# Kernel optimization log

Measured on AMD Instinct MI355X. Metric: run time of the kernel, lower is better.

The kernel has to match this reference:

```python
import jax, jax.numpy as jnp
import numpy as np

B = 32768
K = 8           # moe_num_experts
LATENT = 256    # latent_dim
COND = 1024     # fusion_hidden_dim
HID = 128       # moe_expert_hidden_dim
EIN = LATENT + COND + 1  # expert input dim = 1281


def setup_inputs() -> dict:
    key = jax.random.key(0)
    ks = jax.random.split(key, 12)
    cond = jax.random.normal(ks[0], (B, COND), dtype=jnp.float32)
    u = jax.random.normal(ks[1], (B, LATENT), dtype=jnp.float32)
    tau = jax.random.uniform(ks[2], (B, 1), dtype=jnp.float32)
    # posterior gate: positive, sums to 1 over K (realistic p_hat)
    p_raw = jax.random.uniform(ks[3], (B, K), dtype=jnp.float32)
    p_hat = p_raw / jnp.sum(p_raw, axis=-1, keepdims=True)
    s = 0.02
    W1 = jax.random.normal(ks[4], (K, EIN, HID), dtype=jnp.float32) * s
    b1 = jnp.zeros((K, HID), dtype=jnp.float32)
    W2 = jax.random.normal(ks[5], (K, HID, HID), dtype=jnp.float32) * s
    b2 = jnp.zeros((K, HID), dtype=jnp.float32)
    W3 = jax.random.normal(ks[6], (K, HID, LATENT), dtype=jnp.float32) * s
    b3 = jnp.zeros((K, LATENT), dtype=jnp.float32)
    return {"cond": cond, "u": u, "tau": tau, "p_hat": p_hat,
            "W1": W1, "b1": b1, "W2": W2, "b2": b2, "W3": W3, "b3": b3}


def reference(cond, u, tau, p_hat, W1, b1, W2, b2, W3, b3):
    # Training path: gate = p_hat (no smooth switching, no running gate).
    x = jnp.concatenate([u, cond, tau], axis=-1)           # (B, EIN)
    h = jax.nn.silu(jnp.einsum('bd,kdh->bkh', x, W1) + b1) # (B, K, HID)
    h = jax.nn.silu(jnp.einsum('bkh,khg->bkg', h, W2) + b2)
    v_experts = jnp.einsum('bkg,kgl->bkl', h, W3) + b3     # (B, K, LATENT)
    v = jnp.einsum('bk,bkl->bl', p_hat, v_experts)         # (B, LATENT)
    return v
```

## Files before the change

kernel.cpp:

```cpp
#include <hip/hip_runtime.h>
#include <stdint.h>

typedef unsigned short u16;
typedef __attribute__((ext_vector_type(8))) short short8;
typedef __attribute__((ext_vector_type(4))) float f32x4;
typedef __attribute__((ext_vector_type(4))) uint32_t u32x4;

#define KEXP   8
#define LATENT 256
#define CONDD  1024
#define HID    128
#define EIN    1281
#define EINP   1344
#define NCH    21
#define NTOT   1024
#define BROWS  32768

__device__ __forceinline__ u16 f2bf(float x) {
  uint32_t v = __float_as_uint(x);
  v += 0x7fffu + ((v >> 16) & 1u);
  return (u16)(v >> 16);
}

__device__ __forceinline__ void async16(const void* g, void* l) {
  __builtin_amdgcn_global_load_lds(
      (const __attribute__((address_space(1))) void*)g,
      (__attribute__((address_space(3))) void*)l, 16, 0, 0);
}

__device__ __forceinline__ float silu(float x) { return x / (1.f + __expf(-x)); }

#define W1_TILES (KEXP * 42 * 4)
#define W2_TILES (KEXP * 4 * 4)
#define W3_TILES (KEXP * 4 * 8)
#define WCONV_TILES (W1_TILES + W2_TILES + W3_TILES)
#define XGRP (BROWS * 168)
#define XBLK (XGRP / 256)

__global__ __launch_bounds__(256)
void prep(const float* __restrict__ W1, const float* __restrict__ W2,
          const float* __restrict__ W3, const float* __restrict__ cond,
          const float* __restrict__ uu, const float* __restrict__ tau,
          u16* __restrict__ W1t, u16* __restrict__ W2t, u16* __restrict__ W3t2,
          u16* __restrict__ Xbf) {
  __shared__ float t[32][33];
  const int bid = blockIdx.x;
  if (bid >= WCONV_TILES) {
    int g = (bid - WCONV_TILES) * 256 + threadIdx.x;
    int row = g / 168;
    int c8  = g - row * 168;
    float f0 = 0.f, f1 = 0.f, f2 = 0.f, f3 = 0.f, f4 = 0.f, f5 = 0.f, f6 = 0.f, f7 = 0.f;
    if (c8 < 32) {
      const float4* p = (const float4*)(uu + (size_t)row * LATENT + c8 * 8);
      float4 a = p[0], b = p[1];
      f0 = a.x; f1 = a.y; f2 = a.z; f3 = a.w; f4 = b.x; f5 = b.y; f6 = b.z; f7 = b.w;
    } else if (c8 < 160) {
      const float4* p = (const float4*)(cond + (size_t)row * CONDD + (c8 - 32) * 8);
      float4 a = p[0], b = p[1];
      f0 = a.x; f1 = a.y; f2 = a.z; f3 = a.w; f4 = b.x; f5 = b.y; f6 = b.z; f7 = b.w;
    } else if (c8 == 160) {
      f0 = tau[row];
    }
    u32x4 pk;
    pk[0] = (uint32_t)f2bf(f0) | ((uint32_t)f2bf(f1) << 16);
    pk[1] = (uint32_t)f2bf(f2) | ((uint32_t)f2bf(f3) << 16);
    pk[2] = (uint32_t)f2bf(f4) | ((uint32_t)f2bf(f5) << 16);
    pk[3] = (uint32_t)f2bf(f6) | ((uint32_t)f2bf(f7) << 16);
    *(u32x4*)(Xbf + (size_t)row * EINP + c8 * 8) = pk;
    return;
  }
  const int tx = threadIdx.x & 31, ty = threadIdx.x >> 5;
  if (bid < W1_TILES) {
    int k = bid / 168, r = bid % 168;
    int d0 = (r / 4) * 32, h0 = (r % 4) * 32;
    const float* src = W1 + (size_t)k * EIN * HID;
    #pragma unroll
    for (int s = 0; s < 4; ++s) {
      int d = d0 + ty + s * 8;
      t[ty + s * 8][tx] = (d < EIN) ? src[(size_t)d * HID + h0 + tx] : 0.f;
    }
    __syncthreads();
    u16* dst = W1t + (size_t)k * HID * EINP;
    #pragma unroll
    for (int s = 0; s < 4; ++s)
      dst[(size_t)(h0 + ty + s * 8) * EINP + d0 + tx] = f2bf(t[tx][ty + s * 8]);
  } else if (bid < W1_TILES + W2_TILES) {
    int j = bid - W1_TILES;
    int k = j / 16, r = j % 16;
    int d0 = (r / 4) * 32, h0 = (r % 4) * 32;
    const float* src = W2 + (size_t)k * HID * HID;
    #pragma unroll
    for (int s = 0; s < 4; ++s)
      t[ty + s * 8][tx] = src[(size_t)(d0 + ty + s * 8) * HID + h0 + tx];
    __syncthreads();
    u16* dst = W2t + (size_t)k * HID * HID;
    #pragma unroll
    for (int s = 0; s < 4; ++s)
      dst[(size_t)(h0 + ty + s * 8) * HID + d0 + tx] = f2bf(t[tx][ty + s * 8]);
  } else {
    int j = bid - W1_TILES - W2_TILES;
    int k = j / 32, r = j % 32;
    int d0 = (r / 8) * 32, h0 = (r % 8) * 32;
    const float* src = W3 + (size_t)k * HID * LATENT;
    #pragma unroll
    for (int s = 0; s < 4; ++s)
      t[ty + s * 8][tx] = src[(size_t)(d0 + ty + s * 8) * LATENT + h0 + tx];
    __syncthreads();
    #pragma unroll
    for (int s = 0; s < 4; ++s)
      W3t2[(size_t)(h0 + ty + s * 8) * NTOT + k * HID + d0 + tx] = f2bf(t[tx][ty + s * 8]);
  }
}

__global__ __launch_bounds__(256, 2)
void h1_fused(const u16* __restrict__ Xbf, const u16* __restrict__ W1t,
              const float* __restrict__ b1, const u16* __restrict__ W2t,
              const float* __restrict__ b2, const float* __restrict__ p_hat,
              u16* __restrict__ H) {
  __shared__ struct {
    union {
      struct { u16 As[2][128 * 64]; u16 Bs[2][128 * 64]; } s;
      struct { u16 As2[128 * 128]; u16 Bs2[2][128 * 64]; } g;
      u16 Cs[128 * 72];
    } u;
    float Ps[128];
  } sm;

  const int tid  = threadIdx.x;
  const int wave = tid >> 6;
  const int lane = tid & 63;
  const int q    = lane >> 4;
  const int ln   = lane & 15;
  const int wm   = wave >> 1, wn = wave & 1;
  const int bid  = blockIdx.x;
  const int mt   = ((bid >> 6) << 3) | (bid & 7);
  const int e    = (bid >> 3) & 7;
  const int m0   = mt * 128;
  const u16* w1k = W1t + (size_t)e * HID * EINP;
  const u16* xtb = Xbf + (size_t)m0 * EINP;

  if (tid < 128) sm.Ps[tid] = p_hat[(size_t)(m0 + tid) * KEXP + e];

  const f32x4 fz = {0.f, 0.f, 0.f, 0.f};
  f32x4 acc[4][4];
  #pragma unroll
  for (int m = 0; m < 4; ++m)
    #pragma unroll
    for (int n = 0; n < 4; ++n) acc[m][n] = fz;

  const int rloc = lane >> 3;
  const int gsw  = lane & 7;
  const int gsrc = gsw ^ rloc;

  auto stage = [&](int d0, int bf) {
    #pragma unroll
    for (int i = 0; i < 4; ++i) {
      int rbase = (wave * 4 + i) * 8;
      async16(xtb + (size_t)(rbase + rloc) * EINP + d0 + gsrc * 8,
              &sm.u.s.As[bf][rbase * 64]);
      async16(w1k + (size_t)(rbase + rloc) * EINP + d0 + gsrc * 8,
              &sm.u.s.Bs[bf][rbase * 64]);
    }
  };
  auto mfma_chunk = [&](int bf) {
    const u16* Ab = sm.u.s.As[bf];
    const u16* Bb = sm.u.s.Bs[bf];
    __builtin_amdgcn_s_setprio(1);
    #pragma unroll
    for (int ks = 0; ks < 2; ++ks) {
      short8 a[4], b[4];
      #pragma unroll
      for (int m = 0; m < 4; ++m) {
        int r = wm * 64 + m * 16 + ln;
        int g = (ks * 4 + q) ^ (r & 7);
        a[m] = *(const short8*)(&Ab[r * 64 + g * 8]);
      }
      #pragma unroll
      for (int n = 0; n < 4; ++n) {
        int c = wn * 64 + n * 16 + ln;
        int g = (ks * 4 + q) ^ (c & 7);
        b[n] = *(const short8*)(&Bb[c * 64 + g * 8]);
      }
      #pragma unroll
      for (int m = 0; m < 4; ++m)
        #pragma unroll
        for (int n = 0; n < 4; ++n)
          acc[m][n] = __builtin_amdgcn_mfma_f32_16x16x32_bf16(a[m], b[n], acc[m][n], 0, 0, 0);
    }
    __builtin_amdgcn_s_setprio(0);
  };

  stage(0, 0);
  asm volatile("s_waitcnt vmcnt(0)" ::: "memory");
  __builtin_amdgcn_s_barrier();
  __builtin_amdgcn_sched_barrier(0);

  #pragma unroll 1
  for (int ic2 = 0; ic2 < 10; ++ic2) {
    const int d = ic2 * 128;
    stage(d + 64, 1);
    mfma_chunk(0);
    asm volatile("s_waitcnt vmcnt(0)" ::: "memory");
    __builtin_amdgcn_s_barrier();
    __builtin_amdgcn_sched_barrier(0);
    stage(d + 128, 0);
    mfma_chunk(1);
    asm volatile("s_waitcnt vmcnt(0)" ::: "memory");
    __builtin_amdgcn_s_barrier();
    __builtin_amdgcn_sched_barrier(0);
  }
  mfma_chunk(0);
  __syncthreads();

  const u16* w2k = W2t + (size_t)e * HID * HID;
  #pragma unroll
  for (int kc = 0; kc < 2; ++kc)
    #pragma unroll
    for (int i = 0; i < 4; ++i) {
      int rbase = (wave * 4 + i) * 8;
      async16(w2k + (size_t)(rbase + rloc) * HID + kc * 64 + gsrc * 8,
              &sm.u.g.Bs2[kc][rbase * 64]);
    }

  #pragma unroll
  for (int n = 0; n < 4; ++n) {
    int cl = wn * 64 + n * 16 + ln;
    float bv = b1[e * HID + cl];
    #pragma unroll
    for (int m = 0; m < 4; ++m)
      #pragma unroll
      for (int r = 0; r < 4; ++r) {
        int row = wm * 64 + m * 16 + q * 4 + r;
        sm.u.g.As2[row * 128 + (((cl >> 3) ^ (row & 7)) << 3) + (cl & 7)] =
            f2bf(silu(acc[m][n][r] + bv));
      }
  }

  f32x4 acc2[4][4];
  #pragma unroll
  for (int m = 0; m < 4; ++m)
    #pragma unroll
    for (int n = 0; n < 4; ++n) acc2[m][n] = fz;

  __syncthreads();

  #pragma unroll
  for (int kc = 0; kc < 2; ++kc) {
    #pragma unroll
    for (int ks = 0; ks < 2; ++ks) {
      short8 a[4], b[4];
      #pragma unroll
      for (int m = 0; m < 4; ++m) {
        int r = wm * 64 + m * 16 + ln;
        int G = kc * 8 + ks * 4 + q;
        int g = (G & 8) | ((G ^ (r & 7)) & 7);
        a[m] = *(const short8*)(&sm.u.g.As2[r * 128 + g * 8]);
      }
      #pragma unroll
      for (int n = 0; n < 4; ++n) {
        int c = wn * 64 + n * 16 + ln;
        int g = (ks * 4 + q) ^ (c & 7);
        b[n] = *(const short8*)(&sm.u.g.Bs2[kc][c * 64 + g * 8]);
      }
      #pragma unroll
      for (int m = 0; m < 4; ++m)
        #pragma unroll
        for (int n = 0; n < 4; ++n)
          acc2[m][n] = __builtin_amdgcn_mfma_f32_16x16x32_bf16(a[m], b[n], acc2[m][n], 0, 0, 0);
    }
  }
  __syncthreads();

  u16* hb = H + (size_t)m0 * NTOT + e * HID;
  #pragma unroll 1
  for (int hf = 0; hf < 2; ++hf) {
    if (wn == hf) {
      #pragma unroll
      for (int n = 0; n < 4; ++n) {
        int cl = n * 16 + ln;
        float bv = b2[e * HID + hf * 64 + cl];
        #pragma unroll
        for (int m = 0; m < 4; ++m)
          #pragma unroll
          for (int r = 0; r < 4; ++r) {
            int row = wm * 64 + m * 16 + q * 4 + r;
            sm.u.Cs[row * 72 + cl] = f2bf(sm.Ps[row] * silu(acc2[m][n][r] + bv));
          }
      }
    }
    __syncthreads();
    #pragma unroll
    for (int i = 0; i < 4; ++i) {
      int lin = tid + i * 256;
      int row = lin >> 3;
      int grp = lin & 7;
      *(u32x4*)(hb + (size_t)row * NTOT + hf * 64 + grp * 8) =
          *(const u32x4*)(&sm.u.Cs[row * 72 + grp * 8]);
    }
    __syncthreads();
  }
}

__global__ __launch_bounds__(256, 2)
void out_gemm(const u16* __restrict__ H, const float* __restrict__ p_hat,
              const u16* __restrict__ W3t2, const float* __restrict__ b3,
              float* __restrict__ out) {
  __shared__ struct {
    u16 As[2][64 * 64];
    u16 Bs[2][128 * 64];
    float Ps[64 * 8];
    float B3s[128 * 8];
  } sm;

  const int tid  = threadIdx.x;
  const int wave = tid >> 6;
  const int lane = tid & 63;
  const int q    = lane >> 4;
  const int ln   = lane & 15;
  const int bid  = blockIdx.x;
  const int mt   = ((bid >> 4) << 3) | (bid & 7);
  const int bn   = (bid >> 3) & 1;
  const int m0   = mt * 64, n0 = bn * 128;

  if (tid < 128) {
    int row = tid >> 1, h = tid & 1;
    *(float4*)(&sm.Ps[row * 8 + h * 4]) = *(const float4*)(p_hat + (size_t)(m0 + row) * KEXP + h * 4);
  }
  #pragma unroll
  for (int i = 0; i < 4; ++i) {
    int k = i * 2 + (tid >> 7);
    int c = tid & 127;
    sm.B3s[c * 8 + k] = b3[k * LATENT + n0 + c];
  }

  const f32x4 fz = {0.f, 0.f, 0.f, 0.f};
  f32x4 acc[4][2];
  #pragma unroll
  for (int m = 0; m < 4; ++m) { acc[m][0] = fz; acc[m][1] = fz; }

  const int rloc = lane >> 3;
  const int gsw  = lane & 7;
  const int gsrc = gsw ^ rloc;

  auto stage = [&](int d0, int bf) {
    #pragma unroll
    for (int i = 0; i < 2; ++i) {
      int rbase = (wave * 2 + i) * 8;
      async16(H + (size_t)(m0 + rbase + rloc) * NTOT + d0 + gsrc * 8,
              &sm.As[bf][rbase * 64]);
    }
    #pragma unroll
    for (int i = 0; i < 4; ++i) {
      int rbase = (wave * 4 + i) * 8;
      async16(W3t2 + (size_t)(n0 + rbase + rloc) * NTOT + d0 + gsrc * 8,
              &sm.Bs[bf][rbase * 64]);
    }
  };
  auto mfma_chunk = [&](int bf) {
    const u16* Ab = sm.As[bf];
    const u16* Bb = sm.Bs[bf];
    __builtin_amdgcn_s_setprio(1);
    #pragma unroll
    for (int ks = 0; ks < 2; ++ks) {
      short8 a[4], b[2];
      #pragma unroll
      for (int m = 0; m < 4; ++m) {
        int r = m * 16 + ln;
        int g = (ks * 4 + q) ^ (r & 7);
        a[m] = *(const short8*)(&Ab[r * 64 + g * 8]);
      }
      #pragma unroll
      for (int n = 0; n < 2; ++n) {
        int c = wave * 32 + n * 16 + ln;
        int g = (ks * 4 + q) ^ (c & 7);
        b[n] = *(const short8*)(&Bb[c * 64 + g * 8]);
      }
      #pragma unroll
      for (int m = 0; m < 4; ++m)
        #pragma unroll
        for (int n = 0; n < 2; ++n)
          acc[m][n] = __builtin_amdgcn_mfma_f32_16x16x32_bf16(a[m], b[n], acc[m][n], 0, 0, 0);
    }
    __builtin_amdgcn_s_setprio(0);
  };

  stage(0, 0);
  asm volatile("s_waitcnt vmcnt(0)" ::: "memory");
  __builtin_amdgcn_s_barrier();
  __builtin_amdgcn_sched_barrier(0);

  #pragma unroll 1
  for (int k2 = 0; k2 < 8; ++k2) {
    const int d = k2 * 128;
    stage(d + 64, 1);
    mfma_chunk(0);
    asm volatile("s_waitcnt vmcnt(0)" ::: "memory");
    __builtin_amdgcn_s_barrier();
    __builtin_amdgcn_sched_barrier(0);
    if (k2 < 7) {
      stage(d + 128, 0);
      mfma_chunk(1);
      asm volatile("s_waitcnt vmcnt(0)" ::: "memory");
      __builtin_amdgcn_s_barrier();
      __builtin_amdgcn_sched_barrier(0);
    }
  }
  mfma_chunk(1);

  #pragma unroll
  for (int n = 0; n < 2; ++n) {
    int col = wave * 32 + n * 16 + ln;
    float4 c0 = *(const float4*)(&sm.B3s[col * 8]);
    float4 c1 = *(const float4*)(&sm.B3s[col * 8 + 4]);
    #pragma unroll
    for (int m = 0; m < 4; ++m)
      #pragma unroll
      for (int r = 0; r < 4; ++r) {
        int row = m * 16 + q * 4 + r;
        float4 p0 = *(const float4*)(&sm.Ps[row * 8]);
        float4 p1 = *(const float4*)(&sm.Ps[row * 8 + 4]);
        float v = acc[m][n][r]
                + p0.x * c0.x + p0.y * c0.y + p0.z * c0.z + p0.w * c0.w
                + p1.x * c1.x + p1.y * c1.y + p1.z * c1.z + p1.w * c1.w;
        out[(size_t)(m0 + row) * LATENT + n0 + col] = v;
      }
  }
}

__global__ __launch_bounds__(256, 4)
void h1_gemm(const float* __restrict__ cond, const float* __restrict__ uu,
             const float* __restrict__ tau, const u16* __restrict__ W1t,
             const float* __restrict__ b1, u16* __restrict__ H1) {
  __shared__ union {
    struct { u16 As[128 * 64]; u16 Bs[128 * 64]; } s;
    u16 Cs[128 * 72];
  } sm;

  const int tid  = threadIdx.x;
  const int wave = tid >> 6;
  const int lane = tid & 63;
  const int q    = lane >> 4;
  const int ln   = lane & 15;
  const int wm   = wave >> 1, wn = wave & 1;
  const int bid  = blockIdx.x;
  const int mt   = ((bid >> 6) << 3) | (bid & 7);
  const int e    = (bid >> 3) & 7;
  const int m0   = mt * 128, n0 = e * 128;
  const u16* w1k = W1t + (size_t)e * HID * EINP;

  const f32x4 fz = {0.f, 0.f, 0.f, 0.f};
  f32x4 acc[4][4];
  #pragma unroll
  for (int m = 0; m < 4; ++m)
    #pragma unroll
    for (int n = 0; n < 4; ++n) acc[m][n] = fz;

  #pragma unroll 1
  for (int ic = 0; ic < NCH; ++ic) {
    const int d0 = ic * 64;
    #pragma unroll
    for (int i = 0; i < 4; ++i) {
      int lin  = tid + i * 256;
      int row  = lin >> 3;
      int gsw  = lin & 7;
      int gsrc = gsw ^ (row & 7);
      int gr   = m0 + row;
      float f0, f1, f2, f3, f4, f5, f6, f7;
      if (d0 < 256) {
        const float4* p = (const float4*)(uu + (size_t)gr * LATENT + d0 + gsrc * 8);
        float4 A = p[0], Bv = p[1];
        f0 = A.x; f1 = A.y; f2 = A.z; f3 = A.w; f4 = Bv.x; f5 = Bv.y; f6 = Bv.z; f7 = Bv.w;
      } else if (d0 < 1280) {
        const float4* p = (const float4*)(cond + (size_t)gr * CONDD + (d0 - 256) + gsrc * 8);
        float4 A = p[0], Bv = p[1];
        f0 = A.x; f1 = A.y; f2 = A.z; f3 = A.w; f4 = Bv.x; f5 = Bv.y; f6 = Bv.z; f7 = Bv.w;
      } else {
        float tv = tau[gr];
        f0 = (gsrc == 0) ? tv : 0.f;
        f1 = f2 = f3 = f4 = f5 = f6 = f7 = 0.f;
      }
      u32x4 pk;
      pk[0] = (uint32_t)f2bf(f0) | ((uint32_t)f2bf(f1) << 16);
      pk[1] = (uint32_t)f2bf(f2) | ((uint32_t)f2bf(f3) << 16);
      pk[2] = (uint32_t)f2bf(f4) | ((uint32_t)f2bf(f5) << 16);
      pk[3] = (uint32_t)f2bf(f6) | ((uint32_t)f2bf(f7) << 16);
      *(u32x4*)(&sm.s.As[row * 64 + gsw * 8]) = pk;
    }
    {
      int rloc = lane >> 3;
      int gsw  = lane & 7;
      int gsrc = gsw ^ rloc;
      #pragma unroll
      for (int i = 0; i < 4; ++i) {
        int rbase = (wave * 4 + i) * 8;
        async16(w1k + (size_t)(rbase + rloc) * EINP + d0 + gsrc * 8,
                &sm.s.Bs[rbase * 64]);
      }
    }
    __syncthreads();
    #pragma unroll
    for (int ks = 0; ks < 2; ++ks) {
      short8 a[4], b[4];
      #pragma unroll
      for (int m = 0; m < 4; ++m) {
        int r = wm * 64 + m * 16 + ln;
        int g = (ks * 4 + q) ^ (r & 7);
        a[m] = *(const short8*)(&sm.s.As[r * 64 + g * 8]);
      }
      #pragma unroll
      for (int n = 0; n < 4; ++n) {
        int c = wn * 64 + n * 16 + ln;
        int g = (ks * 4 + q) ^ (c & 7);
        b[n] = *(const short8*)(&sm.s.Bs[c * 64 + g * 8]);
      }
      #pragma unroll
      for (int m = 0; m < 4; ++m)
        #pragma unroll
        for (int n = 0; n < 4; ++n)
          acc[m][n] = __builtin_amdgcn_mfma_f32_16x16x32_bf16(a[m], b[n], acc[m][n], 0, 0, 0);
    }
    __syncthreads();
  }

  #pragma unroll 1
  for (int hf = 0; hf < 2; ++hf) {
    if (wn == hf) {
      #pragma unroll
      for (int n = 0; n < 4; ++n) {
        int cl = n * 16 + ln;
        float bv = b1[n0 + hf * 64 + cl];
        #pragma unroll
        for (int m = 0; m < 4; ++m)
          #pragma unroll
          for (int r = 0; r < 4; ++r)
            sm.Cs[(wm * 64 + m * 16 + q * 4 + r) * 72 + cl] = f2bf(silu(acc[m][n][r] + bv));
      }
    }
    __syncthreads();
    #pragma unroll
    for (int i = 0; i < 4; ++i) {
      int lin = tid + i * 256;
      int row = lin >> 3;
      int grp = lin & 7;
      *(u32x4*)(H1 + (size_t)(m0 + row) * NTOT + n0 + hf * 64 + grp * 8) =
          *(const u32x4*)(&sm.Cs[row * 72 + grp * 8]);
    }
    __syncthreads();
  }
}

__global__ __launch_bounds__(256, 4)
void h2_gemm(u16* __restrict__ H, const float* __restrict__ p_hat,
             const u16* __restrict__ W2t, const float* __restrict__ b2) {
  __shared__ struct {
    union { struct { u16 As[128 * 64]; u16 Bs[128 * 64]; } s; u16 Cs[128 * 72]; } u;
    float Ps[128];
  } sm;

  const int tid  = threadIdx.x;
  const int wave = tid >> 6;
  const int lane = tid & 63;
  const int q    = lane >> 4;
  const int ln   = lane & 15;
  const int wm   = wave >> 1, wn = wave & 1;
  const int mt   = blockIdx.x >> 3;
  const int e    = blockIdx.x & 7;
  const int row0 = mt * 128;

  if (tid < 128) sm.Ps[tid] = p_hat[(size_t)(row0 + tid) * KEXP + e];

  const u16* w2k = W2t + (size_t)e * HID * HID;
  u16* hb = H + (size_t)row0 * NTOT + e * HID;

  const f32x4 fz = {0.f, 0.f, 0.f, 0.f};
  f32x4 acc[4][4];
  #pragma unroll
  for (int m = 0; m < 4; ++m)
    #pragma unroll
    for (int n = 0; n < 4; ++n) acc[m][n] = fz;

  const int rloc = lane >> 3;
  const int gsw  = lane & 7;
  const int gsrc = gsw ^ rloc;

  #pragma unroll 1
  for (int kc = 0; kc < 2; ++kc) {
    #pragma unroll
    for (int i = 0; i < 4; ++i) {
      int rbase = (wave * 4 + i) * 8;
      async16(hb + (size_t)(rbase + rloc) * NTOT + kc * 64 + gsrc * 8,
              &sm.u.s.As[rbase * 64]);
      async16(w2k + (size_t)(rbase + rloc) * HID + kc * 64 + gsrc * 8,
              &sm.u.s.Bs[rbase * 64]);
    }
    __syncthreads();
    #pragma unroll
    for (int ks = 0; ks < 2; ++ks) {
      short8 a[4], b[4];
      #pragma unroll
      for (int m = 0; m < 4; ++m) {
        int r = wm * 64 + m * 16 + ln;
        int g = (ks * 4 + q) ^ (r & 7);
        a[m] = *(const short8*)(&sm.u.s.As[r * 64 + g * 8]);
      }
      #pragma unroll
      for (int n = 0; n < 4; ++n) {
        int c = wn * 64 + n * 16 + ln;
        int g = (ks * 4 + q) ^ (c & 7);
        b[n] = *(const short8*)(&sm.u.s.Bs[c * 64 + g * 8]);
      }
      #pragma unroll
      for (int m = 0; m < 4; ++m)
        #pragma unroll
        for (int n = 0; n < 4; ++n)
          acc[m][n] = __builtin_amdgcn_mfma_f32_16x16x32_bf16(a[m], b[n], acc[m][n], 0, 0, 0);
    }
    __syncthreads();
  }

  #pragma unroll 1
  for (int hf = 0; hf < 2; ++hf) {
    if (wn == hf) {
      #pragma unroll
      for (int n = 0; n < 4; ++n) {
        int cl = n * 16 + ln;
        float bv = b2[e * HID + hf * 64 + cl];
        #pragma unroll
        for (int m = 0; m < 4; ++m)
          #pragma unroll
          for (int r = 0; r < 4; ++r) {
            int row = wm * 64 + m * 16 + q * 4 + r;
            sm.u.Cs[row * 72 + cl] = f2bf(sm.Ps[row] * silu(acc[m][n][r] + bv));
          }
      }
    }
    __syncthreads();
    #pragma unroll
    for (int i = 0; i < 4; ++i) {
      int lin = tid + i * 256;
      int row = lin >> 3;
      int grp = lin & 7;
      *(u32x4*)(hb + (size_t)row * NTOT + hf * 64 + grp * 8) =
          *(const u32x4*)(&sm.u.Cs[row * 72 + grp * 8]);
    }
    __syncthreads();
  }
}

extern "C" void kernel_launch(void* const* d_in, const int* in_sizes, int n_in,
                              void* d_out, int out_size, void* d_ws, size_t ws_size,
                              hipStream_t stream) {
  const float* cond  = (const float*)d_in[0];
  const float* u     = (const float*)d_in[1];
  const float* tau   = (const float*)d_in[2];
  const float* p_hat = (const float*)d_in[3];
  const float* W1    = (const float*)d_in[4];
  const float* b1    = (const float*)d_in[5];
  const float* W2    = (const float*)d_in[6];
  const float* b2    = (const float*)d_in[7];
  const float* W3    = (const float*)d_in[8];
  const float* b3    = (const float*)d_in[9];
  float* out = (float*)d_out;

  const size_t N1 = (size_t)KEXP * HID * EINP;
  const size_t N2 = (size_t)KEXP * HID * HID;
  const size_t N3 = (size_t)LATENT * NTOT;
  const size_t NH = (size_t)BROWS * NTOT;
  const size_t NX = (size_t)BROWS * EINP;

  u16* W1t  = (u16*)d_ws;
  u16* W2t  = W1t + N1;
  u16* W3t2 = W2t + N2;
  u16* H    = W3t2 + N3;

  if (ws_size >= (N1 + N2 + N3 + NH + NX) * sizeof(u16)) {
    u16* Xbf = H + NH;
    prep<<<WCONV_TILES + XBLK, 256, 0, stream>>>(W1, W2, W3, cond, u, tau,
                                                 W1t, W2t, W3t2, Xbf);
    h1_fused<<<2048, 256, 0, stream>>>(Xbf, W1t, b1, W2t, b2, p_hat, H);
    out_gemm<<<1024, 256, 0, stream>>>(H, p_hat, W3t2, b3, out);
  } else if (ws_size >= (N1 + N2 + N3 + NH) * sizeof(u16)) {
    prep<<<WCONV_TILES, 256, 0, stream>>>(W1, W2, W3, cond, u, tau,
                                          W1t, W2t, W3t2, (u16*)nullptr);
    h1_gemm<<<2048, 256, 0, stream>>>(cond, u, tau, W1t, b1, H);
    h2_gemm<<<2048, 256, 0, stream>>>(H, p_hat, W2t, b2);
    out_gemm<<<1024, 256, 0, stream>>>(H, p_hat, W3t2, b3, out);
  }
}
```

Measured before the change: 431.7 us.

## Deepen async prefetch pipelines with triple buffering and partial vmcnt waits

```diff
diff --git a/kernel.cpp b/kernel.cpp
--- a/kernel.cpp
+++ b/kernel.cpp
@@ -117,13 +117,10 @@
               const float* __restrict__ b1, const u16* __restrict__ W2t,
               const float* __restrict__ b2, const float* __restrict__ p_hat,
               u16* __restrict__ H) {
-  __shared__ struct {
-    union {
-      struct { u16 As[2][128 * 64]; u16 Bs[2][128 * 64]; } s;
-      struct { u16 As2[128 * 128]; u16 Bs2[2][128 * 64]; } g;
-      u16 Cs[128 * 72];
-    } u;
-    float Ps[128];
+  __shared__ union {
+    struct { u16 As[3][8192]; u16 Bs[2][8192]; } s;
+    struct { u16 As2[16384]; u16 Bs2[2][8192]; } g;
+    u16 Cs[128 * 72];
   } sm;
 
   const int tid  = threadIdx.x;
@@ -139,8 +136,6 @@
   const u16* w1k = W1t + (size_t)e * HID * EINP;
   const u16* xtb = Xbf + (size_t)m0 * EINP;
 
-  if (tid < 128) sm.Ps[tid] = p_hat[(size_t)(m0 + tid) * KEXP + e];
-
   const f32x4 fz = {0.f, 0.f, 0.f, 0.f};
   f32x4 acc[4][4];
   #pragma unroll
@@ -152,19 +147,20 @@
   const int gsw  = lane & 7;
   const int gsrc = gsw ^ rloc;
 
-  auto stage = [&](int d0, int bf) {
-    #pragma unroll
-    for (int i = 0; i < 4; ++i) {
-      int rbase = (wave * 4 + i) * 8;
-      async16(xtb + (size_t)(rbase + rloc) * EINP + d0 + gsrc * 8,
-              &sm.u.s.As[bf][rbase * 64]);
-      async16(w1k + (size_t)(rbase + rloc) * EINP + d0 + gsrc * 8,
-              &sm.u.s.Bs[bf][rbase * 64]);
-    }
-  };
-  auto mfma_chunk = [&](int bf) {
-    const u16* Ab = sm.u.s.As[bf];
-    const u16* Bb = sm.u.s.Bs[bf];
+#define H1_SA(d0, buf) { \
+  _Pragma("unroll") \
+  for (int i_ = 0; i_ < 4; ++i_) { \
+    int rb_ = (wave * 4 + i_) * 8; \
+    async16(xtb + (size_t)(rb_ + rloc) * EINP + (d0) + gsrc * 8, &sm.s.As[buf][rb_ * 64]); \
+  } }
+#define H1_SB(d0, buf) { \
+  _Pragma("unroll") \
+  for (int i_ = 0; i_ < 4; ++i_) { \
+    int rb_ = (wave * 4 + i_) * 8; \
+    async16(w1k + (size_t)(rb_ + rloc) * EINP + (d0) + gsrc * 8, &sm.s.Bs[buf][rb_ * 64]); \
+  } }
+
+  auto mfma_chunk = [&](const u16* Ab, const u16* Bb) {
     __builtin_amdgcn_s_setprio(1);
     #pragma unroll
     for (int ks = 0; ks < 2; ++ks) {
@@ -190,26 +186,39 @@
     __builtin_amdgcn_s_setprio(0);
   };
 
-  stage(0, 0);
-  asm volatile("s_waitcnt vmcnt(0)" ::: "memory");
+#define H1_CH(trel, ac, bc, bp, ap, vm) \
+  H1_SB(db + ((trel) + 1) * 64, bp); \
+  H1_SA(db + ((trel) + 2) * 64, ap); \
+  mfma_chunk(sm.s.As[ac], sm.s.Bs[bc]); \
+  asm volatile("s_waitcnt vmcnt(" #vm ")" ::: "memory"); \
+  __builtin_amdgcn_s_barrier(); \
+  __builtin_amdgcn_sched_barrier(0);
+
+  H1_SA(0, 0); H1_SB(0, 0); H1_SA(64, 1);
+  asm volatile("s_waitcnt vmcnt(4)" ::: "memory");
   __builtin_amdgcn_s_barrier();
   __builtin_amdgcn_sched_barrier(0);
 
   #pragma unroll 1
-  for (int ic2 = 0; ic2 < 10; ++ic2) {
-    const int d = ic2 * 128;
-    stage(d + 64, 1);
-    mfma_chunk(0);
+  for (int j = 0; j < 3; ++j) {
+    const int db = j * 384;
+    H1_CH(0, 0, 0, 1, 2, 4)
+    H1_CH(1, 1, 1, 0, 0, 4)
+    H1_CH(2, 2, 0, 1, 1, 4)
+    H1_CH(3, 0, 1, 0, 2, 4)
+    H1_CH(4, 1, 0, 1, 0, 4)
+    H1_CH(5, 2, 1, 0, 1, 4)
+  }
+  {
+    const int db = 1152;
+    H1_CH(0, 0, 0, 1, 2, 4)
+    H1_SB(db + 128, 0);
+    mfma_chunk(sm.s.As[1], sm.s.Bs[1]);
     asm volatile("s_waitcnt vmcnt(0)" ::: "memory");
     __builtin_amdgcn_s_barrier();
     __builtin_amdgcn_sched_barrier(0);
-    stage(d + 128, 0);
-    mfma_chunk(1);
-    asm volatile("s_waitcnt vmcnt(0)" ::: "memory");
-    __builtin_amdgcn_s_barrier();
-    __builtin_amdgcn_sched_barrier(0);
-  }
-  mfma_chunk(0);
+    mfma_chunk(sm.s.As[2], sm.s.Bs[0]);
+  }
   __syncthreads();
 
   const u16* w2k = W2t + (size_t)e * HID * HID;
@@ -219,8 +228,15 @@
     for (int i = 0; i < 4; ++i) {
       int rbase = (wave * 4 + i) * 8;
       async16(w2k + (size_t)(rbase + rloc) * HID + kc * 64 + gsrc * 8,
-              &sm.u.g.Bs2[kc][rbase * 64]);
-    }
+              &sm.g.Bs2[kc][rbase * 64]);
+    }
+
+  float pr[4][4];
+  #pragma unroll
+  for (int m = 0; m < 4; ++m)
+    #pragma unroll
+    for (int r = 0; r < 4; ++r)
+      pr[m][r] = p_hat[(size_t)(m0 + wm * 64 + m * 16 + q * 4 + r) * KEXP + e];
 
   #pragma unroll
   for (int n = 0; n < 4; ++n) {
@@ -231,7 +247,7 @@
       #pragma unroll
       for (int r = 0; r < 4; ++r) {
         int row = wm * 64 + m * 16 + q * 4 + r;
-        sm.u.g.As2[row * 128 + (((cl >> 3) ^ (row & 7)) << 3) + (cl & 7)] =
+        sm.g.As2[row * 128 + (((cl >> 3) ^ (row & 7)) << 3) + (cl & 7)] =
             f2bf(silu(acc[m][n][r] + bv));
       }
   }
@@ -254,13 +270,13 @@
         int r = wm * 64 + m * 16 + ln;
         int G = kc * 8 + ks * 4 + q;
         int g = (G & 8) | ((G ^ (r & 7)) & 7);
-        a[m] = *(const short8*)(&sm.u.g.As2[r * 128 + g * 8]);
+        a[m] = *(const short8*)(&sm.g.As2[r * 128 + g * 8]);
       }
       #pragma unroll
       for (int n = 0; n < 4; ++n) {
         int c = wn * 64 + n * 16 + ln;
         int g = (ks * 4 + q) ^ (c & 7);
-        b[n] = *(const short8*)(&sm.u.g.Bs2[kc][c * 64 + g * 8]);
+        b[n] = *(const short8*)(&sm.g.Bs2[kc][c * 64 + g * 8]);
       }
       #pragma unroll
       for (int m = 0; m < 4; ++m)
@@ -284,7 +300,7 @@
           #pragma unroll
           for (int r = 0; r < 4; ++r) {
             int row = wm * 64 + m * 16 + q * 4 + r;
-            sm.u.Cs[row * 72 + cl] = f2bf(sm.Ps[row] * silu(acc2[m][n][r] + bv));
+            sm.Cs[row * 72 + cl] = f2bf(pr[m][r] * silu(acc2[m][n][r] + bv));
           }
       }
     }
@@ -295,10 +311,13 @@
       int row = lin >> 3;
       int grp = lin & 7;
       *(u32x4*)(hb + (size_t)row * NTOT + hf * 64 + grp * 8) =
-          *(const u32x4*)(&sm.u.Cs[row * 72 + grp * 8]);
-    }
-    __syncthreads();
-  }
+          *(const u32x4*)(&sm.Cs[row * 72 + grp * 8]);
+    }
+    __syncthreads();
+  }
+#undef H1_SA
+#undef H1_SB
+#undef H1_CH
 }
 
 __global__ __launch_bounds__(256, 2)
@@ -306,8 +325,8 @@
               const u16* __restrict__ W3t2, const float* __restrict__ b3,
               float* __restrict__ out) {
   __shared__ struct {
-    u16 As[2][64 * 64];
-    u16 Bs[2][128 * 64];
+    u16 As[3][4096];
+    u16 Bs[3][8192];
     float Ps[64 * 8];
     float B3s[128 * 8];
   } sm;
@@ -342,23 +361,20 @@
   const int gsw  = lane & 7;
   const int gsrc = gsw ^ rloc;
 
-  auto stage = [&](int d0, int bf) {
-    #pragma unroll
-    for (int i = 0; i < 2; ++i) {
-      int rbase = (wave * 2 + i) * 8;
-      async16(H + (size_t)(m0 + rbase + rloc) * NTOT + d0 + gsrc * 8,
-              &sm.As[bf][rbase * 64]);
-    }
-    #pragma unroll
-    for (int i = 0; i < 4; ++i) {
-      int rbase = (wave * 4 + i) * 8;
-      async16(W3t2 + (size_t)(n0 + rbase + rloc) * NTOT + d0 + gsrc * 8,
-              &sm.Bs[bf][rbase * 64]);
-    }
-  };
-  auto mfma_chunk = [&](int bf) {
-    const u16* Ab = sm.As[bf];
-    const u16* Bb = sm.Bs[bf];
+#define OG_SA(d0, buf) { \
+  _Pragma("unroll") \
+  for (int i_ = 0; i_ < 2; ++i_) { \
+    int rb_ = (wave * 2 + i_) * 8; \
+    async16(H + (size_t)(m0 + rb_ + rloc) * NTOT + (d0) + gsrc * 8, &sm.As[buf][rb_ * 64]); \
+  } }
+#define OG_SB(d0, buf) { \
+  _Pragma("unroll") \
+  for (int i_ = 0; i_ < 4; ++i_) { \
+    int rb_ = (wave * 4 + i_) * 8; \
+    async16(W3t2 + (size_t)(n0 + rb_ + rloc) * NTOT + (d0) + gsrc * 8, &sm.Bs[buf][rb_ * 64]); \
+  } }
+
+  auto mfma_chunk = [&](const u16* Ab, const u16* Bb) {
     __builtin_amdgcn_s_setprio(1);
     #pragma unroll
     for (int ks = 0; ks < 2; ++ks) {
@@ -384,28 +400,37 @@
     __builtin_amdgcn_s_setprio(0);
   };
 
-  stage(0, 0);
-  asm volatile("s_waitcnt vmcnt(0)" ::: "memory");
+#define OG_CH(trel, ac, ap) \
+  OG_SB(db + ((trel) + 2) * 64, ap); \
+  OG_SA(db + ((trel) + 2) * 64, ap); \
+  mfma_chunk(sm.As[ac], sm.Bs[ac]); \
+  asm volatile("s_waitcnt vmcnt(6)" ::: "memory"); \
+  __builtin_amdgcn_s_barrier(); \
+  __builtin_amdgcn_sched_barrier(0);
+
+  OG_SA(0, 0); OG_SB(0, 0);
+  OG_SA(64, 1); OG_SB(64, 1);
+  asm volatile("s_waitcnt vmcnt(6)" ::: "memory");
   __builtin_amdgcn_s_barrier();
   __builtin_amdgcn_sched_barrier(0);
 
   #pragma unroll 1
-  for (int k2 = 0; k2 < 8; ++k2) {
-    const int d = k2 * 128;
-    stage(d + 64, 1);
-    mfma_chunk(0);
+  for (int j = 0; j < 4; ++j) {
+    const int db = j * 192;
+    OG_CH(0, 0, 2)
+    OG_CH(1, 1, 0)
+    OG_CH(2, 2, 1)
+  }
+  {
+    const int db = 768;
+    OG_CH(0, 0, 2)
+    OG_CH(1, 1, 0)
+    mfma_chunk(sm.As[2], sm.Bs[2]);
     asm volatile("s_waitcnt vmcnt(0)" ::: "memory");
     __builtin_amdgcn_s_barrier();
     __builtin_amdgcn_sched_barrier(0);
-    if (k2 < 7) {
-      stage(d + 128, 0);
-      mfma_chunk(1);
-      asm volatile("s_waitcnt vmcnt(0)" ::: "memory");
-      __builtin_amdgcn_s_barrier();
-      __builtin_amdgcn_sched_barrier(0);
-    }
-  }
-  mfma_chunk(1);
+    mfma_chunk(sm.As[0], sm.Bs[0]);
+  }
 
   #pragma unroll
   for (int n = 0; n < 2; ++n) {
@@ -425,6 +450,9 @@
         out[(size_t)(m0 + row) * LATENT + n0 + col] = v;
       }
   }
+#undef OG_SA
+#undef OG_SB
+#undef OG_CH
 }
 
 __global__ __launch_bounds__(256, 4)
```

Result: faster. 403.7 us (-6.5%).
